# Kernel optimization log

Hardware: AMD Instinct MI355X
Metric: run time of the kernel (lower is better)

Reference implementation:

```python
import jax, jax.numpy as jnp
import numpy as np

B, N, F_IN, H, L, C = 64, 512, 21, 64, 3, 9
NEG_INF = -jnp.inf


def setup_inputs() -> dict:
    key = jax.random.key(0)
    ks = jax.random.split(key, 24)
    s = lambda shape, k, scale=0.05: jax.random.normal(ks[k], shape, dtype=jnp.float32) * scale
    return {
        "node_features": jax.random.normal(ks[0], (B, N, F_IN), dtype=jnp.float32),
        "adjacency": jax.random.bernoulli(ks[1], 0.05, (B, N, N)).astype(jnp.float32),
        "node_mask": jnp.ones((B, N), dtype=bool),
        "We": s((F_IN, H), 2), "be": jnp.zeros((H,), jnp.float32),
        "Wl": s((L, H, H), 3), "a_src": s((L, H), 4), "a_dst": s((L, H), 5),
        "gamma": jnp.ones((L, H), jnp.float32), "beta": jnp.zeros((L, H), jnp.float32),
        "P1": s((H, H), 6), "pb1": jnp.zeros((H,), jnp.float32),
        "P2": s((H,), 7), "pb2": jnp.zeros((), jnp.float32),
        "C1": s((H, H), 8), "cb1": jnp.zeros((H,), jnp.float32),
        "C2": s((H, C), 9), "cb2": jnp.zeros((C,), jnp.float32),
    }


def _layernorm(x, g, b, eps=1e-5):
    mu = x.mean(-1, keepdims=True)
    var = ((x - mu) ** 2).mean(-1, keepdims=True)
    return (x - mu) * jax.lax.rsqrt(var + eps) * g + b


def reference(node_features, adjacency, node_mask, We, be, Wl, a_src, a_dst,
              gamma, beta, P1, pb1, P2, pb2, C1, cb1, C2, cb2):
    # node embedding (dropout = identity in eval)
    h = jax.nn.relu(node_features @ We + be)  # [B,N,H]
    adj_zero = adjacency == 0
    for l in range(L):
        hW = h @ Wl[l]                                  # [B,N,H]
        attn = hW @ a_src[l]                            # [B,N] src scores
        attn = attn[:, :, None] + (hW @ a_dst[l])[:, None, :]  # [B,N,N]
        attn = jax.nn.leaky_relu(attn, 0.2)
        attn = jnp.where(adj_zero, NEG_INF, attn)
        attn = jnp.nan_to_num(jax.nn.softmax(attn, axis=-1), nan=0.0)
        h = _layernorm(h + attn @ hW, gamma[l], beta[l])
    # attention pooling
    pa = jnp.tanh(h @ P1 + pb1) @ P2 + pb2              # [B,N]
    pa = jnp.where(node_mask, pa, NEG_INF)
    pa = jnp.nan_to_num(jax.nn.softmax(pa, axis=-1), nan=0.0)
    g = jnp.einsum('bn,bnh->bh', pa, h)                 # [B,H]
    return jax.nn.relu(g @ C1 + cb1) @ C2 + cb2         # [B,C]
```

## Files before the change

### kernel.cpp

```cpp
#include <hip/hip_runtime.h>


#define WS_H     0
#define WS_HWA   2097152
#define WS_HWB   4194304
#define WS_SA    6291456
#define WS_TA    6324224
#define WS_SB    6356992
#define WS_TB    6389760
#define WS_PA    6422528
#define WS_DEG   6455296
#define WS_LIST_BYTES 25952256

typedef const __attribute__((address_space(1))) unsigned int gu32;
typedef __attribute__((address_space(3))) unsigned int lu32;

__device__ __forceinline__ void gl_lds16(const float* g, float* l) {
  __builtin_amdgcn_global_load_lds((gu32*)g, (lu32*)l, 16, 0, 0);
}

template <int CTRL>
__device__ __forceinline__ float dpp_add(float v) {
  int x = __builtin_amdgcn_update_dpp(0, __float_as_int(v), CTRL, 0xf, 0xf, true);
  return v + __int_as_float(x);
}
__device__ __forceinline__ float wtot(float v) {
  v = dpp_add<0x111>(v);
  v = dpp_add<0x112>(v);
  v = dpp_add<0x114>(v);
  v = dpp_add<0x118>(v);
  v = dpp_add<0x142>(v);
  v = dpp_add<0x143>(v);
  return __int_as_float(__builtin_amdgcn_readlane(__float_as_int(v), 63));
}
__device__ __forceinline__ float bcastf(float v, int l) {
  return __int_as_float(__builtin_amdgcn_readlane(__float_as_int(v), l));
}

__device__ __forceinline__ float wsum(float v) {
#pragma unroll
  for (int o = 32; o; o >>= 1) v += __shfl_xor(v, o, 64);
  return v;
}
__device__ __forceinline__ float wmax(float v) {
#pragma unroll
  for (int o = 32; o; o >>= 1) v = fmaxf(v, __shfl_xor(v, o, 64));
  return v;
}

__global__ __launch_bounds__(512, 4) void k_embed_hw(
    const float* __restrict__ x, const float* __restrict__ We,
    const float* __restrict__ be, const float* __restrict__ adj,
    const float* __restrict__ W0, const float* __restrict__ asrc,
    const float* __restrict__ adst,
    float* __restrict__ h, int* __restrict__ deg,
    unsigned short* __restrict__ nlist,
    float* __restrict__ hW, float* __restrict__ s, float* __restrict__ t) {
  __shared__ float lw[64 * 64];
  int tid = threadIdx.x, lane = tid & 63, wv = tid >> 6;
  int blk = blockIdx.x;
  int xcd = blk & 7, i = blk >> 3;
  int b = xcd * 8 + (i & 7), sub = i >> 3;
  int rb = b * 512 + sub * 32 + wv * 4;
#pragma unroll
  for (int k = 0; k < 2; ++k)
    *(float4*)&lw[k * 2048 + tid * 4] = *(const float4*)&W0[k * 2048 + tid * 4];
  float wreg[21];
#pragma unroll
  for (int f = 0; f < 21; ++f) wreg[f] = We[f * 64 + lane];
  float bev = be[lane];
  unsigned long long lmask = (1ull << lane) - 1ull;
  float4 a0[4], a1[4];
#pragma unroll
  for (int r = 0; r < 4; ++r) {
    const float4* ar = (const float4*)(adj + (size_t)(rb + r) * 512);
    a0[r] = ar[lane];
    a1[r] = ar[64 + lane];
  }
  float hst[4];
#pragma unroll
  for (int r = 0; r < 4; ++r) {
    int row = rb + r;
    const float* xr = x + (size_t)row * 21;
    float acc = bev;
#pragma unroll
    for (int f = 0; f < 21; ++f) acc = fmaf(xr[f], wreg[f], acc);
    acc = fmaxf(acc, 0.0f);
    h[(size_t)row * 64 + lane] = acc;
    hst[r] = acc;
    float comp[8] = {a0[r].x, a0[r].y, a0[r].z, a0[r].w,
                     a1[r].x, a1[r].y, a1[r].z, a1[r].w};
    int cnt = 0;
#pragma unroll
    for (int c = 0; c < 8; ++c) {
      bool on = comp[c] != 0.0f;
      unsigned long long m = __ballot(on);
      if (on) {
        int pos = cnt + __popcll(m & lmask);
        int col = (c < 4) ? (lane * 4 + c) : (256 + lane * 4 + (c - 4));
        if (pos < 64)
          nlist[(size_t)row * 64 + pos] = (unsigned short)col;
      }
      cnt += __popcll(m);
    }
    if (lane == 0) deg[row] = cnt < 64 ? cnt : 64;
  }
  __syncthreads();
  float av = asrc[lane], dv = adst[lane];
  float acc[4] = {};
#pragma unroll 8
  for (int c = 0; c < 64; ++c) {
    float wrow = lw[c * 64 + lane];
#pragma unroll
    for (int r = 0; r < 4; ++r)
      acc[r] = fmaf(bcastf(hst[r], c), wrow, acc[r]);
  }
#pragma unroll
  for (int r = 0; r < 4; ++r) {
    int row = rb + r;
    hW[(size_t)row * 64 + lane] = acc[r];
    float ps = wtot(acc[r] * av);
    float pt = wtot(acc[r] * dv);
    if (lane == 0) { s[row] = ps; t[row] = pt; }
  }
}

template <int MODE>
__global__ __launch_bounds__(1024) void k_layer(
    float* __restrict__ h, const float* __restrict__ hWin,
    const float* __restrict__ sIn, const float* __restrict__ tIn,
    const int* __restrict__ deg, const unsigned short* __restrict__ nlist,
    const float* __restrict__ gamma, const float* __restrict__ beta,
    const float* __restrict__ Wn, const float* __restrict__ v1,
    const float* __restrict__ v2,
    float* __restrict__ hWout, float* __restrict__ sOut,
    float* __restrict__ tOut) {
  __shared__ float hlds[512 * 64];
  __shared__ float lw[64 * 64];
  __shared__ float tlds[512];
  int tid = threadIdx.x, lane = tid & 63, wv = tid >> 6;
  int blk = blockIdx.x;
  int b = (blk & 7) * 8 + ((blk >> 3) & 7);
  int sub = blk >> 6;
  int rb = b * 512 + sub * 128 + wv * 8;

  unsigned short jr[8]; float sir[8], hrr[8]; int dgr[8];
#pragma unroll
  for (int r = 0; r < 8; ++r) {
    int row = rb + r;
    jr[r] = nlist[(size_t)row * 64 + lane];
    sir[r] = sIn[row];
    hrr[r] = h[(size_t)row * 64 + lane];
    dgr[r] = deg[row];
  }
  *(float4*)&lw[tid * 4] = *(const float4*)&Wn[tid * 4];
  const float* tb = tIn + ((size_t)b << 9);
  if (tid < 128) *(float4*)&tlds[tid * 4] = *(const float4*)&tb[tid * 4];
  {
    const char* src = (const char*)(hWin + ((size_t)b << 9) * 64);
    char* dst = (char*)hlds;
#pragma unroll
    for (int c = 0; c < 8; ++c) {
      int off = wv * 8192 + c * 1024;
      gl_lds16((const float*)(src + off + lane * 16), (float*)(dst + off));
    }
  }
  __syncthreads();

  float gm = gamma[lane], bt = beta[lane];
  float hst[8];
#pragma unroll
  for (int r = 0; r < 8; ++r) {
    int dgs = __builtin_amdgcn_readfirstlane(dgr[r]);
    bool act = lane < dgs;
    int jm = act ? (int)jr[r] : 0;
    float tv = act ? tlds[jm] : 0.0f;
    float e = sir[r] + tv;
    e = e > 0.0f ? e : 0.2f * e;
    float wj = act ? __expf(e) : 0.0f;
    float dsum = wtot(wj);
    float acc0 = 0.0f, acc1 = 0.0f;
    int dg8 = (dgs + 7) & ~7;
    for (int n = 0; n < dg8; n += 8) {
#pragma unroll
      for (int k = 0; k < 8; k += 2) {
        int j0 = __builtin_amdgcn_readlane(jm, n + k);
        int w0 = __builtin_amdgcn_readlane(__float_as_int(wj), n + k);
        int j1 = __builtin_amdgcn_readlane(jm, n + k + 1);
        int w1 = __builtin_amdgcn_readlane(__float_as_int(wj), n + k + 1);
        acc0 = fmaf(__int_as_float(w0), hlds[j0 * 64 + lane], acc0);
        acc1 = fmaf(__int_as_float(w1), hlds[j1 * 64 + lane], acc1);
      }
    }
    float a = dgs > 0 ? (acc0 + acc1) * (1.0f / dsum) : 0.0f;
    float xv = hrr[r] + a;
    float s1 = wtot(xv), s2 = wtot(xv * xv);
    float mu = s1 * 0.015625f;
    float var = fmaf(-mu, mu, s2 * 0.015625f);
    float hn = fmaf((xv - mu) * rsqrtf(var + 1e-5f), gm, bt);
    h[(size_t)(rb + r) * 64 + lane] = hn;
    hst[r] = hn;
  }
  if (MODE == 0) {
    float av = v1[lane], dv = v2[lane];
    float acc[8] = {};
#pragma unroll 8
    for (int c = 0; c < 64; ++c) {
      float wrow = lw[c * 64 + lane];
#pragma unroll
      for (int r = 0; r < 8; ++r)
        acc[r] = fmaf(bcastf(hst[r], c), wrow, acc[r]);
    }
#pragma unroll
    for (int r = 0; r < 8; ++r) {
      int row = rb + r;
      hWout[(size_t)row * 64 + lane] = acc[r];
      float ps = wtot(acc[r] * av);
      float pt = wtot(acc[r] * dv);
      if (lane == 0) { sOut[row] = ps; tOut[row] = pt; }
    }
  } else {
    float b1 = v1[lane], p2 = v2[lane];
    float acc[8] = {};
#pragma unroll 8
    for (int c = 0; c < 64; ++c) {
      float wrow = lw[c * 64 + lane];
#pragma unroll
      for (int r = 0; r < 8; ++r)
        acc[r] = fmaf(bcastf(hst[r], c), wrow, acc[r]);
    }
#pragma unroll
    for (int r = 0; r < 8; ++r) {
      int row = rb + r;
      float p = wtot(tanhf(acc[r] + b1) * p2);
      if (lane == 0) sOut[row] = p;
    }
  }
}

__global__ __launch_bounds__(512) void k_pool(const float* __restrict__ h,
    const float* __restrict__ pa, const float* __restrict__ C1,
    const float* __restrict__ cb1, const float* __restrict__ C2,
    const float* __restrict__ cb2, float* __restrict__ out) {
  __shared__ float red[8];
  __shared__ float gpart[8][64];
  __shared__ float gl[64], rl[64];
  int b = ((blockIdx.x & 7) << 3) | (blockIdx.x >> 3);
  int tid = threadIdx.x, lane = tid & 63, wv = tid >> 6;
  float v = pa[b * 512 + tid];
  float m = wmax(v);
  if (lane == 0) red[wv] = m;
  __syncthreads();
  float bm = red[0];
#pragma unroll
  for (int w = 1; w < 8; ++w) bm = fmaxf(bm, red[w]);
  float e = __expf(v - bm);
  float sm = wsum(e);
  __syncthreads();
  if (lane == 0) red[wv] = sm;
  __syncthreads();
  float bs = 0.0f;
#pragma unroll
  for (int w = 0; w < 8; ++w) bs += red[w];
  float p = e / bs;
  const float* hb = h + ((size_t)b * 512) * 64;
  float g = 0.0f;
#pragma unroll
  for (int l = 0; l < 64; ++l) {
    float pj = __shfl(p, l, 64);
    g = fmaf(pj, hb[(size_t)(wv * 64 + l) * 64 + lane], g);
  }
  gpart[wv][lane] = g;
  __syncthreads();
  if (wv == 0) {
    float gg = 0.0f;
#pragma unroll
    for (int w = 0; w < 8; ++w) gg += gpart[w][lane];
    gl[lane] = gg;
    float rr = cb1[lane];
#pragma unroll
    for (int j = 0; j < 64; ++j) rr = fmaf(gl[j], C1[j * 64 + lane], rr);
    rr = fmaxf(rr, 0.0f);
    rl[lane] = rr;
    if (lane < 9) {
      float o = cb2[lane];
#pragma unroll
      for (int k = 0; k < 64; ++k) o = fmaf(rl[k], C2[k * 9 + lane], o);
      out[b * 9 + lane] = o;
    }
  }
}

extern "C" void kernel_launch(void* const* d_in, const int* in_sizes, int n_in,
                              void* d_out, int out_size, void* d_ws, size_t ws_size,
                              hipStream_t stream) {
  const float* x    = (const float*)d_in[0];
  const float* adj  = (const float*)d_in[1];
  const float* We   = (const float*)d_in[3];
  const float* be   = (const float*)d_in[4];
  const float* Wl   = (const float*)d_in[5];
  const float* asrc = (const float*)d_in[6];
  const float* adst = (const float*)d_in[7];
  const float* gamma= (const float*)d_in[8];
  const float* beta = (const float*)d_in[9];
  const float* P1   = (const float*)d_in[10];
  const float* pb1  = (const float*)d_in[11];
  const float* P2   = (const float*)d_in[12];
  const float* C1   = (const float*)d_in[14];
  const float* cb1  = (const float*)d_in[15];
  const float* C2   = (const float*)d_in[16];
  const float* cb2  = (const float*)d_in[17];
  float* out = (float*)d_out;

  float* ws  = (float*)d_ws;
  float* h   = ws + WS_H;
  float* hwA = ws + WS_HWA;
  float* hwB = ws + WS_HWB;
  float* sA  = ws + WS_SA;
  float* tA  = ws + WS_TA;
  float* sB  = ws + WS_SB;
  float* tB  = ws + WS_TB;
  float* pa  = ws + WS_PA;
  int*   deg = (int*)(ws + WS_DEG);
  unsigned short* nlist = (unsigned short*)((char*)d_ws + WS_LIST_BYTES);

  k_embed_hw<<<1024, 512, 0, stream>>>(x, We, be, adj, Wl, asrc, adst,
                                       h, deg, nlist, hwA, sA, tA);
  k_layer<0><<<256, 1024, 0, stream>>>(h, hwA, sA, tA, deg, nlist,
                                       gamma, beta, Wl + 4096,
                                       asrc + 64, adst + 64, hwB, sB, tB);
  k_layer<0><<<256, 1024, 0, stream>>>(h, hwB, sB, tB, deg, nlist,
                                       gamma + 64, beta + 64, Wl + 8192,
                                       asrc + 128, adst + 128, hwA, sA, tA);
  k_layer<1><<<256, 1024, 0, stream>>>(h, hwA, sA, tA, deg, nlist,
                                       gamma + 128, beta + 128, P1, pb1, P2,
                                       nullptr, pa, nullptr);
  k_pool<<<64, 512, 0, stream>>>(h, pa, C1, cb1, C2, cb2, out);
}
```

Measured before the change: 246.7 us.

## Register-tile layer matmul via LDS transpose, pack neighbor index with weight, stage nlist writes

The per-layer 128x64x64 matmul that produced the next hW (or the pooling scores) is restructured. Instead of each wave broadcasting its own rows lane by lane, the normalized rows are transposed into LDS and each thread computes a 2x4 register tile, reading a padded weight matrix. Softmax weights have their low 9 mantissa bits replaced by the neighbor index, so the aggregation loop needs one readlane per neighbor instead of two. This slightly perturbs the weight values, though the denominator is computed from the same truncated weights. The embed kernel also stages neighbor lists in LDS and writes them out as coalesced ushort4 stores.

```diff
diff --git a/kernel.cpp b/kernel.cpp
--- a/kernel.cpp
+++ b/kernel.cpp
@@ -33,6 +33,13 @@
   v = dpp_add<0x143>(v);
   return __int_as_float(__builtin_amdgcn_readlane(__float_as_int(v), 63));
 }
+__device__ __forceinline__ float rsum16d(float v) {
+  v = dpp_add<0x111>(v);
+  v = dpp_add<0x112>(v);
+  v = dpp_add<0x114>(v);
+  v = dpp_add<0x118>(v);
+  return v;
+}
 __device__ __forceinline__ float bcastf(float v, int l) {
   return __int_as_float(__builtin_amdgcn_readlane(__float_as_int(v), l));
 }
@@ -57,6 +64,7 @@
     unsigned short* __restrict__ nlist,
     float* __restrict__ hW, float* __restrict__ s, float* __restrict__ t) {
   __shared__ float lw[64 * 64];
+  __shared__ unsigned short lidx[8][4][64];
   int tid = threadIdx.x, lane = tid & 63, wv = tid >> 6;
   int blk = blockIdx.x;
   int xcd = blk & 7, i = blk >> 3;
@@ -98,12 +106,15 @@
       if (on) {
         int pos = cnt + __popcll(m & lmask);
         int col = (c < 4) ? (lane * 4 + c) : (256 + lane * 4 + (c - 4));
-        if (pos < 64)
-          nlist[(size_t)row * 64 + pos] = (unsigned short)col;
+        if (pos < 64) lidx[wv][r][pos] = (unsigned short)col;
       }
       cnt += __popcll(m);
     }
     if (lane == 0) deg[row] = cnt < 64 ? cnt : 64;
+  }
+  {
+    ushort4 v = *(ushort4*)&lidx[wv][0][lane * 4];
+    *(ushort4*)(nlist + (size_t)rb * 64 + lane * 4) = v;
   }
   __syncthreads();
   float av = asrc[lane], dv = adst[lane];
@@ -136,13 +147,14 @@
     float* __restrict__ hWout, float* __restrict__ sOut,
     float* __restrict__ tOut) {
   __shared__ float hlds[512 * 64];
-  __shared__ float lw[64 * 64];
+  __shared__ float lw[64 * 68];
   __shared__ float tlds[512];
   int tid = threadIdx.x, lane = tid & 63, wv = tid >> 6;
   int blk = blockIdx.x;
   int b = (blk & 7) * 8 + ((blk >> 3) & 7);
   int sub = blk >> 6;
-  int rb = b * 512 + sub * 128 + wv * 8;
+  int base = b * 512 + sub * 128;
+  int rb = base + wv * 8;
 
   unsigned short jr[8]; float sir[8], hrr[8]; int dgr[8];
 #pragma unroll
@@ -153,7 +165,10 @@
     hrr[r] = h[(size_t)row * 64 + lane];
     dgr[r] = deg[row];
   }
-  *(float4*)&lw[tid * 4] = *(const float4*)&Wn[tid * 4];
+  {
+    int rr = tid >> 4, q = tid & 15;
+    *(float4*)&lw[rr * 68 + q * 4] = *(const float4*)&Wn[rr * 64 + q * 4];
+  }
   const float* tb = tIn + ((size_t)b << 9);
   if (tid < 128) *(float4*)&tlds[tid * 4] = *(const float4*)&tb[tid * 4];
   {
@@ -178,20 +193,23 @@
     float e = sir[r] + tv;
     e = e > 0.0f ? e : 0.2f * e;
     float wj = act ? __expf(e) : 0.0f;
-    float dsum = wtot(wj);
+    int bits = __float_as_int(wj) & ~511;
+    int packed = bits | jm;
+    float wq = __int_as_float(bits);
     float acc0 = 0.0f, acc1 = 0.0f;
     int dg8 = (dgs + 7) & ~7;
     for (int n = 0; n < dg8; n += 8) {
 #pragma unroll
       for (int k = 0; k < 8; k += 2) {
-        int j0 = __builtin_amdgcn_readlane(jm, n + k);
-        int w0 = __builtin_amdgcn_readlane(__float_as_int(wj), n + k);
-        int j1 = __builtin_amdgcn_readlane(jm, n + k + 1);
-        int w1 = __builtin_amdgcn_readlane(__float_as_int(wj), n + k + 1);
-        acc0 = fmaf(__int_as_float(w0), hlds[j0 * 64 + lane], acc0);
-        acc1 = fmaf(__int_as_float(w1), hlds[j1 * 64 + lane], acc1);
+        int u0 = __builtin_amdgcn_readlane(packed, n + k);
+        int u1 = __builtin_amdgcn_readlane(packed, n + k + 1);
+        acc0 = fmaf(__int_as_float(u0 & ~511),
+                    hlds[(u0 & 511) * 64 + lane], acc0);
+        acc1 = fmaf(__int_as_float(u1 & ~511),
+                    hlds[(u1 & 511) * 64 + lane], acc1);
       }
     }
+    float dsum = wtot(wq);
     float a = dgs > 0 ? (acc0 + acc1) * (1.0f / dsum) : 0.0f;
     float xv = hrr[r] + a;
     float s1 = wtot(xv), s2 = wtot(xv * xv);
@@ -201,39 +219,47 @@
     h[(size_t)(rb + r) * 64 + lane] = hn;
     hst[r] = hn;
   }
-  if (MODE == 0) {
-    float av = v1[lane], dv = v2[lane];
-    float acc[8] = {};
-#pragma unroll 8
-    for (int c = 0; c < 64; ++c) {
-      float wrow = lw[c * 64 + lane];
-#pragma unroll
-      for (int r = 0; r < 8; ++r)
-        acc[r] = fmaf(bcastf(hst[r], c), wrow, acc[r]);
-    }
-#pragma unroll
-    for (int r = 0; r < 8; ++r) {
-      int row = rb + r;
-      hWout[(size_t)row * 64 + lane] = acc[r];
-      float ps = wtot(acc[r] * av);
-      float pt = wtot(acc[r] * dv);
-      if (lane == 0) { sOut[row] = ps; tOut[row] = pt; }
-    }
-  } else {
-    float b1 = v1[lane], p2 = v2[lane];
-    float acc[8] = {};
-#pragma unroll 8
-    for (int c = 0; c < 64; ++c) {
-      float wrow = lw[c * 64 + lane];
-#pragma unroll
-      for (int r = 0; r < 8; ++r)
-        acc[r] = fmaf(bcastf(hst[r], c), wrow, acc[r]);
-    }
-#pragma unroll
-    for (int r = 0; r < 8; ++r) {
-      int row = rb + r;
-      float p = wtot(tanhf(acc[r] + b1) * p2);
-      if (lane == 0) sOut[row] = p;
+  __syncthreads();
+  float* lhT = hlds;
+#pragma unroll
+  for (int r = 0; r < 8; ++r) lhT[lane * 132 + (wv * 8 + r)] = hst[r];
+  __syncthreads();
+  int tc = tid & 15, tr = tid >> 4;
+  float acc[2][4] = {};
+#pragma unroll 4
+  for (int c = 0; c < 64; ++c) {
+    float2 aa = *(const float2*)&lhT[c * 132 + tr * 2];
+    float4 bb = *(const float4*)&lw[c * 68 + tc * 4];
+    float av2[2] = {aa.x, aa.y};
+    float bv[4] = {bb.x, bb.y, bb.z, bb.w};
+#pragma unroll
+    for (int ii = 0; ii < 2; ++ii)
+#pragma unroll
+      for (int j = 0; j < 4; ++j)
+        acc[ii][j] = fmaf(av2[ii], bv[j], acc[ii][j]);
+  }
+  float p1[4], p2[4];
+#pragma unroll
+  for (int j = 0; j < 4; ++j) { p1[j] = v1[tc * 4 + j]; p2[j] = v2[tc * 4 + j]; }
+#pragma unroll
+  for (int ii = 0; ii < 2; ++ii) {
+    int row = base + tr * 2 + ii;
+    if (MODE == 0) {
+      *(float4*)&hWout[(size_t)row * 64 + tc * 4] =
+          make_float4(acc[ii][0], acc[ii][1], acc[ii][2], acc[ii][3]);
+      float ps = acc[ii][0] * p1[0] + acc[ii][1] * p1[1] +
+                 acc[ii][2] * p1[2] + acc[ii][3] * p1[3];
+      float pt = acc[ii][0] * p2[0] + acc[ii][1] * p2[1] +
+                 acc[ii][2] * p2[2] + acc[ii][3] * p2[3];
+      ps = rsum16d(ps);
+      pt = rsum16d(pt);
+      if (tc == 15) { sOut[row] = ps; tOut[row] = pt; }
+    } else {
+      float p = 0.0f;
+#pragma unroll
+      for (int j = 0; j < 4; ++j) p += tanhf(acc[ii][j] + p1[j]) * p2[j];
+      p = rsum16d(p);
+      if (tc == 15) sOut[row] = p;
     }
   }
 }
```

Measured after the change: 225.6 us. 1.09x faster.
